# Kernel optimization log

Hardware: AMD Instinct MI355X
Metric: run time of the kernel (lower is better)

Reference implementation:

```python
import jax, jax.numpy as jnp
import numpy as np

B, T, C = 4, 4096, 1024
H = 16
NBLOCKS, BSIZE = 32, 128
HD = C // H  # 64


def setup_inputs() -> dict:
    key = jax.random.key(0)
    ks = jax.random.split(key, 8)
    s = 1.0 / np.sqrt(C)
    return {
        "x": jax.random.normal(ks[0], (B, T, C), dtype=jnp.float32),
        "Wq": jax.random.uniform(ks[1], (C, C), jnp.float32, -s, s),
        "bq": jax.random.uniform(ks[2], (C,), jnp.float32, -s, s),
        "Wk": jax.random.uniform(ks[3], (C, C), jnp.float32, -s, s),
        "Wv": jax.random.uniform(ks[4], (C, C), jnp.float32, -s, s),
        "bv": jax.random.uniform(ks[5], (C,), jnp.float32, -s, s),
        "Wo": jax.random.uniform(ks[6], (C, C), jnp.float32, -s, s),
        "bo": jax.random.uniform(ks[7], (C,), jnp.float32, -s, s),
    }


def reference(x, Wq, bq, Wk, Wv, bv, Wo, bo):
    # Linear projections (torch F.linear: x @ W.T + b; key has no bias)
    q = x @ Wq.T + bq
    k = x @ Wk.T
    v = x @ Wv.T + bv

    scale = HD ** (-0.25)
    # reshape to (B, nblocks, bsize, H, head_dim); scale applied to q and k
    q = q.reshape(B, NBLOCKS, BSIZE, H, HD) * scale
    k = k.reshape(B, NBLOCKS, BSIZE, H, HD) * scale
    v = v.reshape(B, NBLOCKS, BSIZE, H, HD)

    # block-local scores: (B, H, nblocks, bsize, bsize)
    qk = jnp.einsum('bnqhd,bnkhd->bhnqk', q, k)
    w = jax.nn.softmax(qk.astype(jnp.float32), axis=-1).astype(q.dtype)
    # attention output: (B, H, nblocks, bsize, head_dim)
    o = jnp.einsum('bhnqk,bnkhd->bhnqd', w, v)
    # -> (B, nblocks, bsize, H, head_dim) -> (B, T, C)
    o = o.transpose(0, 2, 3, 1, 4).reshape(B, T, C)
    return o @ Wo.T + bo
```

## Files before the change

### kernel.cpp

```cpp
#include <hip/hip_runtime.h>
#include <stdint.h>

#define Bb   4
#define Tt   4096
#define Cc   1024
#define Hh   16
#define HDd  64
#define NBn  32
#define BSs  128
#define MTOT (Bb*Tt)

typedef short s16;
typedef __attribute__((ext_vector_type(8))) short  short8;
typedef __attribute__((ext_vector_type(4))) float  f32x4;
typedef __attribute__((ext_vector_type(4))) int    int4v;

__device__ __forceinline__ s16 f2bf(float f) {
  union { float f; uint32_t u; } c; c.f = f;
  return (s16)((c.u + 0x7fffu + ((c.u >> 16) & 1u)) >> 16);
}

typedef const __attribute__((address_space(1))) void* gas_p;
typedef __attribute__((address_space(3))) void*       las_p;
__device__ __forceinline__ void lds16(const void* g, void* l) {
  __builtin_amdgcn_global_load_lds((gas_p)g, (las_p)l, 16, 0, 0);
}

__global__ __launch_bounds__(256) void cvt_x(const float* __restrict__ in, s16* __restrict__ out) {
  int i = blockIdx.x * 256 + threadIdx.x;
  const f32x4* p = (const f32x4*)(in + (size_t)i * 8);
  f32x4 a = p[0], b = p[1];
  short8 o;
  o[0]=f2bf(a[0]); o[1]=f2bf(a[1]); o[2]=f2bf(a[2]); o[3]=f2bf(a[3]);
  o[4]=f2bf(b[0]); o[5]=f2bf(b[1]); o[6]=f2bf(b[2]); o[7]=f2bf(b[3]);
  *(short8*)(out + (size_t)i * 8) = o;
}

__global__ __launch_bounds__(256) void cvt_w(const float* w0, const float* w1,
                                             const float* w2, const float* w3,
                                             s16* o0, s16* o1, s16* o2, s16* o3) {
  int i = blockIdx.x * 256 + threadIdx.x;
  int which = i >> 17;
  int j = i & 131071;
  const float* w = which == 0 ? w0 : which == 1 ? w1 : which == 2 ? w2 : w3;
  s16*         o = which == 0 ? o0 : which == 1 ? o1 : which == 2 ? o2 : o3;
  const f32x4* p = (const f32x4*)(w + (size_t)j * 8);
  f32x4 a = p[0], b = p[1];
  short8 v;
  v[0]=f2bf(a[0]); v[1]=f2bf(a[1]); v[2]=f2bf(a[2]); v[3]=f2bf(a[3]);
  v[4]=f2bf(b[0]); v[5]=f2bf(b[1]); v[6]=f2bf(b[2]); v[7]=f2bf(b[3]);
  *(short8*)(o + (size_t)j * 8) = v;
}

template <bool OUT_BF16, int NX>
__global__ __launch_bounds__(256) void gemm_bt(const s16* __restrict__ A, const s16* __restrict__ Bm,
                                               const float* b0, const float* b1, const float* b2,
                                               void* o0, void* o1, void* o2) {
  __shared__ s16 smem[17408];
  s16* As = smem;
  s16* Bs = smem + 8192;

  const int tid = threadIdx.x;
  const int w = tid >> 6, l = tid & 63;
  const int lr = l & 15, lk = l >> 4;
  const int wr = w >> 1, wc = w & 1;

  const int lid = blockIdx.x;
  const int xcd = lid & 7, sl = lid >> 3;
  const int per_row = NX * 8;
  const int chunk = sl / per_row;
  const int rem = sl - chunk * per_row;
  const int yy = rem / NX;
  const int xx = rem - yy * NX;
  const int mBase = (xcd * 16 + chunk * 8 + yy) * 128;
  const int nBase = xx * 128;

  f32x4 acc[4][4];
#pragma unroll
  for (int i = 0; i < 4; ++i)
#pragma unroll
    for (int j = 0; j < 4; ++j) acc[i][j] = (f32x4){0.f, 0.f, 0.f, 0.f};

  for (int k0 = 0; k0 < Cc; k0 += 64) {
#pragma unroll
    for (int t = 0; t < 4; ++t) {
      int s = t * 256 + tid;
      int r = s >> 3, gp = s & 7;
      int kg = gp ^ (r & 7);
      lds16(A  + (size_t)(mBase + r) * Cc + (k0 + kg * 8), &As[(t * 256 + w * 64) * 8]);
      lds16(Bm + (size_t)(nBase + r) * Cc + (k0 + kg * 8), &Bs[(t * 256 + w * 64) * 8]);
    }
    __syncthreads();

#pragma unroll
    for (int kk = 0; kk < 2; ++kk) {
      short8 af[4], bf[4];
#pragma unroll
      for (int mt = 0; mt < 4; ++mt) {
        int row = wr * 64 + mt * 16 + lr;
        af[mt] = *(const short8*)&As[row * 64 + (((kk * 4 + lk) ^ (row & 7)) * 8)];
      }
#pragma unroll
      for (int nt = 0; nt < 4; ++nt) {
        int row = wc * 64 + nt * 16 + lr;
        bf[nt] = *(const short8*)&Bs[row * 64 + (((kk * 4 + lk) ^ (row & 7)) * 8)];
      }
#pragma unroll
      for (int mt = 0; mt < 4; ++mt)
#pragma unroll
        for (int nt = 0; nt < 4; ++nt)
          acc[mt][nt] = __builtin_amdgcn_mfma_f32_16x16x32_bf16(af[mt], bf[nt], acc[mt][nt], 0, 0, 0);
    }
    __syncthreads();
  }

  if (OUT_BF16) {
    const int seg = nBase >> 10;
    const float* bias = seg == 0 ? b0 : (seg == 1 ? b1 : b2);
    s16* outp = (s16*)(seg == 0 ? o0 : (seg == 1 ? o1 : o2));
    const int colL = nBase & 1023;
    s16* Cs = smem;
#pragma unroll
    for (int nt = 0; nt < 4; ++nt) {
      int col = wc * 64 + nt * 16 + lr;
      float bb = bias ? bias[colL + col] : 0.0f;
#pragma unroll
      for (int mt = 0; mt < 4; ++mt) {
        int row0 = wr * 64 + mt * 16 + lk * 4;
#pragma unroll
        for (int i = 0; i < 4; ++i)
          Cs[(row0 + i) * 136 + col] = f2bf(acc[mt][nt][i] + bb);
      }
    }
    __syncthreads();
#pragma unroll
    for (int t = 0; t < 8; ++t) {
      int s = t * 256 + tid;
      int r = s >> 4, g = s & 15;
      *(short8*)&outp[(size_t)(mBase + r) * 1024 + colL + g * 8] =
          *(const short8*)&Cs[r * 136 + g * 8];
    }
  } else {
    float* outp = (float*)o0;
#pragma unroll
    for (int nt = 0; nt < 4; ++nt) {
      int col = nBase + wc * 64 + nt * 16 + lr;
      float bb = b0[col];
#pragma unroll
      for (int mt = 0; mt < 4; ++mt) {
        int row0 = mBase + wr * 64 + mt * 16 + lk * 4;
#pragma unroll
        for (int i = 0; i < 4; ++i)
          outp[(size_t)(row0 + i) * 1024 + col] = acc[mt][nt][i] + bb;
      }
    }
  }
}

__global__ __launch_bounds__(256) void attn_kernel(const s16* __restrict__ Q, const s16* __restrict__ K,
                                                   const s16* __restrict__ V, s16* __restrict__ O) {
  __shared__ s16   u_qkp[19456];
  __shared__ s16   vsT[64 * 136];
  __shared__ float invSum[128];

  const int tid = threadIdx.x;
  const int w = tid >> 6, l = tid & 63;
  const int lr = l & 15, lk = l >> 4;
  const int bid = blockIdx.x;
  const int b = bid >> 9;
  const int n = (bid >> 4) & 31;
  const int h = bid & 15;
  const size_t tokBase = (size_t)b * Tt + (size_t)n * BSs;
  const int colBase = h * HDd;

  s16* qs = u_qkp;
  s16* ks = u_qkp + 9216;
  s16* P  = u_qkp;

#pragma unroll
  for (int t = 0; t < 4; ++t) {
    int s = t * 256 + tid;
    int r = s >> 3, g = s & 7;
    size_t gidx = (tokBase + r) * Cc + colBase + g * 8;
    int4v  dq = *(const int4v*)&Q[gidx];
    int4v  dk = *(const int4v*)&K[gidx];
    short8 dv = *(const short8*)&V[gidx];
    *(int4v*)&qs[r * 72 + g * 8] = dq;
    *(int4v*)&ks[r * 72 + g * 8] = dk;
    int rg = r >> 3, rl = r & 7;
#pragma unroll
    for (int e = 0; e < 8; ++e) {
      int d = g * 8 + e;
      vsT[d * 136 + ((rg ^ e ^ g) << 3) + rl] = dv[e];
    }
  }
  __syncthreads();

  f32x4 accS[2][8];
#pragma unroll
  for (int mt = 0; mt < 2; ++mt)
#pragma unroll
    for (int nt = 0; nt < 8; ++nt) accS[mt][nt] = (f32x4){0.f, 0.f, 0.f, 0.f};

#pragma unroll
  for (int st = 0; st < 2; ++st) {
    short8 aq[2], bk[8];
#pragma unroll
    for (int mt = 0; mt < 2; ++mt)
      aq[mt] = *(const short8*)&qs[(w * 32 + mt * 16 + lr) * 72 + st * 32 + lk * 8];
#pragma unroll
    for (int nt = 0; nt < 8; ++nt)
      bk[nt] = *(const short8*)&ks[(nt * 16 + lr) * 72 + st * 32 + lk * 8];
#pragma unroll
    for (int mt = 0; mt < 2; ++mt)
#pragma unroll
      for (int nt = 0; nt < 8; ++nt)
        accS[mt][nt] = __builtin_amdgcn_mfma_f32_16x16x32_bf16(aq[mt], bk[nt], accS[mt][nt], 0, 0, 0);
  }

#pragma unroll
  for (int mt = 0; mt < 2; ++mt)
#pragma unroll
    for (int i = 0; i < 4; ++i) {
      float m = accS[mt][0][i];
#pragma unroll
      for (int nt = 1; nt < 8; ++nt) m = fmaxf(m, accS[mt][nt][i]);
      m = fmaxf(m, __shfl_xor(m, 1));
      m = fmaxf(m, __shfl_xor(m, 2));
      m = fmaxf(m, __shfl_xor(m, 4));
      m = fmaxf(m, __shfl_xor(m, 8));
      float sum = 0.f;
#pragma unroll
      for (int nt = 0; nt < 8; ++nt) {
        float p = __expf((accS[mt][nt][i] - m) * 0.125f);
        sum += p;
        accS[mt][nt][i] = p;
      }
      sum += __shfl_xor(sum, 1);
      sum += __shfl_xor(sum, 2);
      sum += __shfl_xor(sum, 4);
      sum += __shfl_xor(sum, 8);
      if (lr == 0) invSum[w * 32 + mt * 16 + lk * 4 + i] = 1.0f / sum;
    }
  __syncthreads();

#pragma unroll
  for (int mt = 0; mt < 2; ++mt)
#pragma unroll
    for (int nt = 0; nt < 8; ++nt)
#pragma unroll
      for (int i = 0; i < 4; ++i)
        P[(w * 32 + mt * 16 + lk * 4 + i) * 152 + nt * 16 + lr] = f2bf(accS[mt][nt][i]);
  __syncthreads();

  f32x4 accO[2][4];
#pragma unroll
  for (int mt = 0; mt < 2; ++mt)
#pragma unroll
    for (int nt = 0; nt < 4; ++nt) accO[mt][nt] = (f32x4){0.f, 0.f, 0.f, 0.f};

#pragma unroll
  for (int st = 0; st < 4; ++st) {
    short8 ap[2], bv[4];
#pragma unroll
    for (int mt = 0; mt < 2; ++mt)
      ap[mt] = *(const short8*)&P[(w * 32 + mt * 16 + lr) * 152 + st * 32 + lk * 8];
#pragma unroll
    for (int nt = 0; nt < 4; ++nt) {
      int d = nt * 16 + lr;
      bv[nt] = *(const short8*)&vsT[d * 136 + ((((st * 4 + lk) ^ (d & 7) ^ (d >> 3))) << 3)];
    }
#pragma unroll
    for (int mt = 0; mt < 2; ++mt)
#pragma unroll
      for (int nt = 0; nt < 4; ++nt)
        accO[mt][nt] = __builtin_amdgcn_mfma_f32_16x16x32_bf16(ap[mt], bv[nt], accO[mt][nt], 0, 0, 0);
  }

#pragma unroll
  for (int mt = 0; mt < 2; ++mt)
#pragma unroll
    for (int nt = 0; nt < 4; ++nt)
#pragma unroll
      for (int i = 0; i < 4; ++i) {
        int rl = w * 32 + mt * 16 + lk * 4 + i;
        int d = nt * 16 + lr;
        float v = accO[mt][nt][i] * invSum[rl];
        O[(tokBase + rl) * Cc + colBase + d] = f2bf(v);
      }
}

extern "C" void kernel_launch(void* const* d_in, const int* in_sizes, int n_in,
                              void* d_out, int out_size, void* d_ws, size_t ws_size,
                              hipStream_t stream) {
  const float* x  = (const float*)d_in[0];
  const float* Wq = (const float*)d_in[1];
  const float* bq = (const float*)d_in[2];
  const float* Wk = (const float*)d_in[3];
  const float* Wv = (const float*)d_in[4];
  const float* bv = (const float*)d_in[5];
  const float* Wo = (const float*)d_in[6];
  const float* bo = (const float*)d_in[7];

  if (ws_size < (size_t)75497472) return;
  char* ws = (char*)d_ws;
  s16* xb  = (s16*)(ws);
  s16* wqb = (s16*)(ws + 33554432);
  s16* wkb = (s16*)(ws + 35651584);
  s16* wvb = (s16*)(ws + 37748736);
  s16* wob = (s16*)(ws + 39845888);
  s16* Qb  = (s16*)(ws + 41943040);
  s16* Kb  = (s16*)((char*)d_out);
  s16* Vb  = (s16*)((char*)d_out + 33554432);

  cvt_x<<<8192, 256, 0, stream>>>(x, xb);
  cvt_w<<<2048, 256, 0, stream>>>(Wq, Wk, Wv, Wo, wqb, wkb, wvb, wob);

  gemm_bt<true, 24><<<24 * 128, 256, 0, stream>>>(xb, wqb, bq, nullptr, bv, Qb, Kb, Vb);

  attn_kernel<<<Bb * NBn * Hh, 256, 0, stream>>>(Qb, Kb, Vb, Qb);

  gemm_bt<false, 8><<<8 * 128, 256, 0, stream>>>(Qb, wob, bo, bo, bo, (float*)d_out, nullptr, nullptr);
}
```

Before: 344.7 us.

## Replace 128x128 GEMM with double-buffered 256x256 tile, 512-thread kernel

Both projection GEMMs move from 128x128 tiles with 4 waves to 256x256 tiles with 8 waves. Each wave computes a 128x64 sub-tile. Global-to-LDS loads are double-buffered so the next K tile is fetched while MFMAs run on the current one. The kernel uses raw s_barrier, s_setprio and sched_barrier to interleave loads and compute. The bf16 epilogue is staged through LDS in two halves. The aim is to raise arithmetic intensity per LDS byte and hide load latency. In exchange it uses 128KB of LDS per block and launches far fewer blocks, 768 and 256, which may leave CUs idle on the output projection.

New measurement: 317.0 us. 1.09x faster.

```diff
diff --git a/kernel.cpp b/kernel.cpp
--- a/kernel.cpp
+++ b/kernel.cpp
@@ -52,66 +52,87 @@
   *(short8*)(o + (size_t)j * 8) = v;
 }
 
-template <bool OUT_BF16, int NX>
-__global__ __launch_bounds__(256) void gemm_bt(const s16* __restrict__ A, const s16* __restrict__ Bm,
-                                               const float* b0, const float* b1, const float* b2,
-                                               void* o0, void* o1, void* o2) {
-  __shared__ s16 smem[17408];
-  s16* As = smem;
-  s16* Bs = smem + 8192;
+template <bool OUT_BF16, int NXT>
+__global__ __launch_bounds__(512, 2) void gemm256(const s16* __restrict__ Ag, const s16* __restrict__ Bg,
+                                                  const float* b0, const float* b1, const float* b2,
+                                                  void* o0, void* o1, void* o2) {
+  __shared__ s16 smem[65536];
 
   const int tid = threadIdx.x;
   const int w = tid >> 6, l = tid & 63;
   const int lr = l & 15, lk = l >> 4;
-  const int wr = w >> 1, wc = w & 1;
+  const int wm = w >> 2, wn = w & 3;
 
   const int lid = blockIdx.x;
-  const int xcd = lid & 7, sl = lid >> 3;
-  const int per_row = NX * 8;
-  const int chunk = sl / per_row;
-  const int rem = sl - chunk * per_row;
-  const int yy = rem / NX;
-  const int xx = rem - yy * NX;
-  const int mBase = (xcd * 16 + chunk * 8 + yy) * 128;
-  const int nBase = xx * 128;
-
-  f32x4 acc[4][4];
-#pragma unroll
-  for (int i = 0; i < 4; ++i)
+  const int xcd = lid & 7, s0 = lid >> 3;
+  const int my = xcd * 8 + s0 / NXT;
+  const int nx = s0 - (s0 / NXT) * NXT;
+  const int mBase = my * 256, nBase = nx * 256;
+
+  f32x4 acc[8][4];
+#pragma unroll
+  for (int i = 0; i < 8; ++i)
 #pragma unroll
     for (int j = 0; j < 4; ++j) acc[i][j] = (f32x4){0.f, 0.f, 0.f, 0.f};
 
-  for (int k0 = 0; k0 < Cc; k0 += 64) {
-#pragma unroll
-    for (int t = 0; t < 4; ++t) {
-      int s = t * 256 + tid;
-      int r = s >> 3, gp = s & 7;
-      int kg = gp ^ (r & 7);
-      lds16(A  + (size_t)(mBase + r) * Cc + (k0 + kg * 8), &As[(t * 256 + w * 64) * 8]);
-      lds16(Bm + (size_t)(nBase + r) * Cc + (k0 + kg * 8), &Bs[(t * 256 + w * 64) * 8]);
-    }
-    __syncthreads();
-
-#pragma unroll
-    for (int kk = 0; kk < 2; ++kk) {
-      short8 af[4], bf[4];
-#pragma unroll
-      for (int mt = 0; mt < 4; ++mt) {
-        int row = wr * 64 + mt * 16 + lr;
-        af[mt] = *(const short8*)&As[row * 64 + (((kk * 4 + lk) ^ (row & 7)) * 8)];
-      }
-#pragma unroll
-      for (int nt = 0; nt < 4; ++nt) {
-        int row = wc * 64 + nt * 16 + lr;
-        bf[nt] = *(const short8*)&Bs[row * 64 + (((kk * 4 + lk) ^ (row & 7)) * 8)];
-      }
-#pragma unroll
-      for (int mt = 0; mt < 4; ++mt)
+  auto stage_tile = [&](int slot, int k0) {
+    s16* Asl = smem + slot * 16384;
+    s16* Bsl = smem + 32768 + slot * 16384;
+#pragma unroll
+    for (int L = 0; L < 4; ++L) {
+      int s = L * 512 + tid;
+      int r = s >> 3;
+      int kg = (s & 7) ^ (r & 7);
+      int wbase = (L * 512 + (tid & ~63)) * 8;
+      lds16(Ag + (size_t)(mBase + r) * Cc + (k0 + kg * 8), Asl + wbase);
+      lds16(Bg + (size_t)(nBase + r) * Cc + (k0 + kg * 8), Bsl + wbase);
+    }
+  };
+
+  stage_tile(0, 0);
+  __syncthreads();
+
+  for (int kt = 0; kt < 16; ++kt) {
+    const int c = kt & 1;
+    const s16* Asc = smem + c * 16384;
+    const s16* Bsc = smem + 32768 + c * 16384;
+
+    if (kt < 15) stage_tile(c ^ 1, (kt + 1) * 64);
+
+    short8 bk[4][2];
+#pragma unroll
+    for (int nt = 0; nt < 4; ++nt)
+#pragma unroll
+      for (int kk = 0; kk < 2; ++kk) {
+        int row = wn * 64 + nt * 16 + lr;
+        bk[nt][kk] = *(const short8*)&Bsc[row * 64 + (((kk * 4 + lk) ^ (lr & 7)) * 8)];
+      }
+
+#pragma unroll
+    for (int q = 0; q < 4; ++q) {
+      short8 af[2][2];
+#pragma unroll
+      for (int mt2 = 0; mt2 < 2; ++mt2)
+#pragma unroll
+        for (int kk = 0; kk < 2; ++kk) {
+          int row = wm * 128 + (q * 2 + mt2) * 16 + lr;
+          af[mt2][kk] = *(const short8*)&Asc[row * 64 + (((kk * 4 + lk) ^ (lr & 7)) * 8)];
+        }
+      __builtin_amdgcn_s_setprio(1);
+#pragma unroll
+      for (int mt2 = 0; mt2 < 2; ++mt2)
 #pragma unroll
         for (int nt = 0; nt < 4; ++nt)
-          acc[mt][nt] = __builtin_amdgcn_mfma_f32_16x16x32_bf16(af[mt], bf[nt], acc[mt][nt], 0, 0, 0);
-    }
-    __syncthreads();
+#pragma unroll
+          for (int kk = 0; kk < 2; ++kk)
+            acc[q * 2 + mt2][nt] = __builtin_amdgcn_mfma_f32_16x16x32_bf16(
+                af[mt2][kk], bk[nt][kk], acc[q * 2 + mt2][nt], 0, 0, 0);
+      __builtin_amdgcn_s_setprio(0);
+      if (q == 3) asm volatile("s_waitcnt vmcnt(0)" ::: "memory");
+      __builtin_amdgcn_sched_barrier(0);
+      asm volatile("s_barrier" ::: "memory");
+      __builtin_amdgcn_sched_barrier(0);
+    }
   }
 
   if (OUT_BF16) {
@@ -121,34 +142,40 @@
     const int colL = nBase & 1023;
     s16* Cs = smem;
 #pragma unroll
-    for (int nt = 0; nt < 4; ++nt) {
-      int col = wc * 64 + nt * 16 + lr;
-      float bb = bias ? bias[colL + col] : 0.0f;
-#pragma unroll
-      for (int mt = 0; mt < 4; ++mt) {
-        int row0 = wr * 64 + mt * 16 + lk * 4;
-#pragma unroll
-        for (int i = 0; i < 4; ++i)
-          Cs[(row0 + i) * 136 + col] = f2bf(acc[mt][nt][i] + bb);
-      }
-    }
-    __syncthreads();
-#pragma unroll
-    for (int t = 0; t < 8; ++t) {
-      int s = t * 256 + tid;
-      int r = s >> 4, g = s & 15;
-      *(short8*)&outp[(size_t)(mBase + r) * 1024 + colL + g * 8] =
-          *(const short8*)&Cs[r * 136 + g * 8];
+    for (int h = 0; h < 2; ++h) {
+      if (wm == h) {
+#pragma unroll
+        for (int nt = 0; nt < 4; ++nt) {
+          int col = wn * 64 + nt * 16 + lr;
+          float bb = bias ? bias[colL + col] : 0.0f;
+#pragma unroll
+          for (int mt = 0; mt < 8; ++mt) {
+            int r0 = mt * 16 + lk * 4;
+#pragma unroll
+            for (int i = 0; i < 4; ++i)
+              Cs[(r0 + i) * 264 + col] = f2bf(acc[mt][nt][i] + bb);
+          }
+        }
+      }
+      __syncthreads();
+#pragma unroll
+      for (int t = 0; t < 8; ++t) {
+        int s2 = t * 512 + tid;
+        int r = s2 >> 5, g = s2 & 31;
+        *(short8*)&outp[(size_t)(mBase + h * 128 + r) * 1024 + colL + g * 8] =
+            *(const short8*)&Cs[r * 264 + g * 8];
+      }
+      __syncthreads();
     }
   } else {
     float* outp = (float*)o0;
 #pragma unroll
     for (int nt = 0; nt < 4; ++nt) {
-      int col = nBase + wc * 64 + nt * 16 + lr;
+      int col = nBase + wn * 64 + nt * 16 + lr;
       float bb = b0[col];
 #pragma unroll
-      for (int mt = 0; mt < 4; ++mt) {
-        int row0 = mBase + wr * 64 + mt * 16 + lk * 4;
+      for (int mt = 0; mt < 8; ++mt) {
+        int row0 = mBase + wm * 128 + mt * 16 + lk * 4;
 #pragma unroll
         for (int i = 0; i < 4; ++i)
           outp[(size_t)(row0 + i) * 1024 + col] = acc[mt][nt][i] + bb;
@@ -316,9 +343,9 @@
   cvt_x<<<8192, 256, 0, stream>>>(x, xb);
   cvt_w<<<2048, 256, 0, stream>>>(Wq, Wk, Wv, Wo, wqb, wkb, wvb, wob);
 
-  gemm_bt<true, 24><<<24 * 128, 256, 0, stream>>>(xb, wqb, bq, nullptr, bv, Qb, Kb, Vb);
+  gemm256<true, 12><<<8 * 8 * 12, 512, 0, stream>>>(xb, wqb, bq, nullptr, bv, Qb, Kb, Vb);
 
   attn_kernel<<<Bb * NBn * Hh, 256, 0, stream>>>(Qb, Kb, Vb, Qb);
 
-  gemm_bt<false, 8><<<8 * 128, 256, 0, stream>>>(Qb, wob, bo, bo, bo, (float*)d_out, nullptr, nullptr);
-}
+  gemm256<false, 4><<<8 * 8 * 4, 512, 0, stream>>>(Qb, wob, bo, bo, bo, (float*)d_out, nullptr, nullptr);
+}
```
